# Kernel tuning notes

Hardware: AMD Instinct MI355X
Metric: run time of the kernel (lower is better)

Reference implementation:

```python
import jax, jax.numpy as jnp
import numpy as np

NC = 65536   # candidate centers across FPN levels (single image)
NP = 1024    # proposal boxes == points
D = 256      # points_feat_dim
C = 256      # in_channels (query/key dim)
START_LEVEL = 3
NEG = -1e30


def setup_inputs() -> dict:
    key = jax.random.key(0)
    ks = jax.random.split(key, 9)
    # centers: [y, x, size, stride]; stride in {8,16,32,64,128} -> lvl 0..4
    lvl = jax.random.randint(ks[0], (NC,), 0, 5)
    stride = (2.0 ** (lvl + START_LEVEL)).astype(jnp.float32)
    yx = jax.random.uniform(ks[1], (NC, 2), minval=0.0, maxval=1024.0)
    centers = jnp.concatenate([yx, stride[:, None], stride[:, None]], axis=1)
    # boxes: [x1, y1, x2, y2]
    x1y1 = jax.random.uniform(ks[2], (NP, 2), minval=0.0, maxval=900.0)
    wh = jax.random.uniform(ks[3], (NP, 2), minval=64.0, maxval=256.0)
    boxes = jnp.concatenate([x1y1, x1y1 + wh], axis=1)
    points_feat = jax.random.normal(ks[4], (NP, D), dtype=jnp.float32)
    box_feat = jax.random.normal(ks[5], (NC, D), dtype=jnp.float32)
    Wq = jax.random.normal(ks[6], (D, C), dtype=jnp.float32) / np.sqrt(D).astype(np.float32)
    bq = jnp.zeros((C,), dtype=jnp.float32)
    Wk = jax.random.normal(ks[7], (D, C), dtype=jnp.float32) / np.sqrt(D).astype(np.float32)
    bk = jnp.zeros((C,), dtype=jnp.float32)
    scales = 1.0 + 0.1 * jax.random.normal(ks[8], (5,), dtype=jnp.float32)
    return dict(points_feat=points_feat, box_feat=box_feat, centers=centers,
                boxes=boxes, Wq=Wq, bq=bq, Wk=Wk, bk=bk, scales=scales)


def reference(points_feat, box_feat, centers, boxes, Wq, bq, Wk, bk, scales):
    # geometry -> containment mask [NC, NP] (center c inside box p)
    coord = centers[:, :2] + jnp.floor_divide(centers[:, 2:3], 2.0)  # [NC,2]
    ys, xs = coord[:, 0], coord[:, 1]
    l = xs[:, None] - boxes[None, :, 0]
    t = ys[:, None] - boxes[None, :, 1]
    r = boxes[None, :, 2] - xs[:, None]
    b = boxes[None, :, 3] - ys[:, None]
    mask = jnp.minimum(jnp.minimum(l, t), jnp.minimum(r, b)) > 0     # [NC,NP]

    stride = centers[:, 3]
    lvl = (jnp.log2(stride) - START_LEVEL).astype(jnp.int32)         # [NC] in 0..4
    w = scales[lvl]                                                  # per-level scale

    query = points_feat @ Wq + bq                                    # [NP,C]
    keyf = (box_feat * w[:, None]) @ Wk + bk                         # [NC,C]

    sim = jnp.clip(keyf @ query.T, -50.0, 50.0)                      # [NC,NP]
    logits = jnp.where(mask, sim, NEG)
    attn = jax.nn.softmax(logits, axis=0)
    attn = jnp.where(mask, attn, 0.0)                                # zero out invalid
    merge = attn.T @ box_feat                                        # [NP,D]
    return points_feat + merge
```

## Files before the change

### kernel.cpp

```cpp
#include <hip/hip_runtime.h>

typedef unsigned short ushort_t;
typedef _Float16 half8 __attribute__((ext_vector_type(8)));
typedef short short8 __attribute__((ext_vector_type(8)));
typedef float floatx4 __attribute__((ext_vector_type(4)));

#define NCC 65536
#define NPP 1024
#define DD 256
#define NCHUNK 64
#define VROW 36
#define VTILE_B (256 * VROW * 2)

static __device__ __forceinline__ ushort_t f2h_bits(float x) {
  _Float16 h = (_Float16)x;
  return __builtin_bit_cast(ushort_t, h);
}
static __device__ __forceinline__ ushort_t f2bf_bits(float x) {
  unsigned u = __builtin_bit_cast(unsigned, x);
  unsigned r = (u + 0x7FFFu + ((u >> 16) & 1u)) >> 16;
  return (ushort_t)r;
}
static __device__ __forceinline__ ushort_t f2bf_cast(float x) {
  __bf16 h = (__bf16)x;
  return __builtin_bit_cast(ushort_t, h);
}

static __device__ __forceinline__ void dma16(const void* g, void* l) {
  __builtin_amdgcn_global_load_lds((const __attribute__((address_space(1))) unsigned int*)g,
                                   (__attribute__((address_space(3))) unsigned int*)l, 16, 0, 0);
}

static __device__ __forceinline__ short8 mk_s8(uint2 lo, uint2 hi) {
  uint4 u;
  u.x = lo.x; u.y = lo.y; u.z = hi.x; u.w = hi.y;
  return __builtin_bit_cast(short8, u);
}

__global__ __launch_bounds__(256) void wt_prep(const float* __restrict__ Wq,
                                               const float* __restrict__ Wk,
                                               ushort_t* __restrict__ WqT,
                                               ushort_t* __restrict__ WkT) {
  __shared__ __align__(16) ushort_t lt[64][80];
  const float* W = blockIdx.y ? Wk : Wq;
  ushort_t* WT = blockIdx.y ? WkT : WqT;
  const int k0 = ((int)blockIdx.x & 3) * 64, n0 = ((int)blockIdx.x >> 2) * 64;
  const int t = threadIdx.x;
#pragma unroll
  for (int i = 0; i < 4; i++) {
    int f = t + 256 * i;
    int k = f >> 4, j = (f & 15) * 4;
    const float4 v = *(const float4*)&W[(size_t)(k0 + k) * DD + n0 + j];
    lt[j + 0][k] = f2h_bits(v.x);
    lt[j + 1][k] = f2h_bits(v.y);
    lt[j + 2][k] = f2h_bits(v.z);
    lt[j + 3][k] = f2h_bits(v.w);
  }
  __syncthreads();
#pragma unroll
  for (int i = 0; i < 2; i++) {
    int f = t + 256 * i;
    int nl = f >> 3, grp = f & 7;
    int n = n0 + nl;
    int kp = k0 + ((grp ^ (n & 7)) * 8);
    *(uint4*)&WT[(size_t)n * DD + kp] = *(const uint4*)&lt[nl][grp * 8];
  }
}

__global__ __launch_bounds__(256) void prep_gemm(
    const float* __restrict__ box_feat, const float* __restrict__ points_feat,
    const float* __restrict__ centers, const float* __restrict__ scales,
    const ushort_t* __restrict__ WqT, const ushort_t* __restrict__ WkT,
    const float* __restrict__ bq, const float* __restrict__ bk,
    ushort_t* __restrict__ q_out, ushort_t* __restrict__ kf_out,
    ushort_t* __restrict__ vTb, float2* __restrict__ xy) {
  __shared__ __align__(16) ushort_t lds_a[64][264];
  __shared__ __align__(16) ushort_t lds_b[64 * 256];
  __shared__ __align__(16) ushort_t lds_o[64][72];
  __shared__ float lds_s[64];

  const int t = threadIdx.x;
  const bool isQ = (blockIdx.x >= (NCC / 64));
  const int row0 = isQ ? ((int)blockIdx.x - NCC / 64) * 64 : (int)blockIdx.x * 64;
  const float* In = isQ ? points_feat : box_feat;
  const ushort_t* WT = isQ ? WqT : WkT;
  const float* Bi = isQ ? bq : bk;
  ushort_t* Out = isQ ? q_out : kf_out;
  const int swz = isQ ? 0 : 7;

  const int r0 = t >> 4;
  const int cj = (t & 15) * 4;
  float4 vld[4][4];
#pragma unroll
  for (int p = 0; p < 4; ++p)
#pragma unroll
    for (int i2 = 0; i2 < 4; ++i2)
      vld[p][i2] = *(const float4*)&In[(size_t)(row0 + r0 + 16 * i2) * DD + p * 64 + cj];

  if (t < 64) {
    float s = 1.0f;
    if (!isQ) {
      int c = row0 + t;
      float stride = centers[c * 4 + 3];
      int lvl = (int)(log2f(stride) + 0.5f) - 3;
      lvl = lvl < 0 ? 0 : (lvl > 4 ? 4 : lvl);
      s = scales[lvl];
      float hf = floorf(centers[c * 4 + 2] * 0.5f);
      xy[c] = make_float2(centers[c * 4 + 1] + hf, centers[c * 4 + 0] + hf);
    }
    lds_s[t] = s;
  }
  __syncthreads();

  float sc[4];
#pragma unroll
  for (int i2 = 0; i2 < 4; ++i2) sc[i2] = lds_s[r0 + 16 * i2];

  {
    ushort_t(*lt)[72] = lds_o;
#pragma unroll
    for (int p = 0; p < 4; ++p) {
#pragma unroll
      for (int i2 = 0; i2 < 4; ++i2) {
        const float4 v = vld[p][i2];
        const int row = r0 + 16 * i2;
        const float s = sc[i2];
        ushort_t h0 = f2h_bits(v.x * s), h1 = f2h_bits(v.y * s);
        ushort_t h2 = f2h_bits(v.z * s), h3 = f2h_bits(v.w * s);
        *(uint2*)&lds_a[row][p * 64 + cj] =
            make_uint2((unsigned)h0 | ((unsigned)h1 << 16), (unsigned)h2 | ((unsigned)h3 << 16));
        if (!isQ) {
          lt[cj + 0][row] = f2bf_bits(v.x);
          lt[cj + 1][row] = f2bf_bits(v.y);
          lt[cj + 2][row] = f2bf_bits(v.z);
          lt[cj + 3][row] = f2bf_bits(v.w);
        }
      }
      if (!isQ) {
        __syncthreads();
#pragma unroll
        for (int i3 = 0; i3 < 2; i3++) {
          int f = t + 256 * i3;
          int d = f >> 3, jg = f & 7;
          int tile = (row0 >> 5) + (jg >> 2);
          size_t ob = (size_t)tile * (256 * VROW) + (size_t)(p * 64 + d) * VROW + (jg & 3) * 8;
          const uint2* src = (const uint2*)&lt[d][jg * 8];
          *(uint2*)&vTb[ob] = src[0];
          *(uint2*)&vTb[ob + 4] = src[1];
        }
        __syncthreads();
      }
    }
  }

  const int w = t >> 6, lane = t & 63, qd = lane >> 4, n = lane & 15;
  const int sw8 = (n & 7) * 8;

  for (int g = 0; g < 4; ++g) {
    __syncthreads();
#pragma unroll
    for (int j = 0; j < 8; ++j) {
      int sg = w * 8 + j;
      dma16(&WT[(size_t)g * 64 * DD + sg * 512 + lane * 8], &lds_b[sg * 512 + lane * 8]);
    }
    __syncthreads();

    floatx4 acc[4] = {};
#pragma unroll
    for (int s = 0; s < 8; s++) {
      half8 af = __builtin_bit_cast(half8, *(const uint4*)&lds_a[w * 16 + n][s * 32 + qd * 8]);
      int off = (s * 32 + qd * 8) ^ sw8;
#pragma unroll
      for (int nt = 0; nt < 4; ++nt) {
        half8 bf = __builtin_bit_cast(half8, *(const uint4*)&lds_b[(nt * 16 + n) * 256 + off]);
        acc[nt] = __builtin_amdgcn_mfma_f32_16x16x32_f16(af, bf, acc[nt], 0, 0, 0);
      }
    }
#pragma unroll
    for (int nt = 0; nt < 4; ++nt) {
      float b = Bi[g * 64 + nt * 16 + n];
#pragma unroll
      for (int r = 0; r < 4; r++) lds_o[w * 16 + qd * 4 + r][nt * 16 + n] = f2h_bits(acc[nt][r] + b);
    }
    __syncthreads();
#pragma unroll
    for (int i = 0; i < 2; i++) {
      int idx = t * 2 + i;
      int r = idx >> 3, grp = idx & 7;
      uint4 v = *(const uint4*)&lds_o[r][grp * 8];
      int grpS = grp ^ (swz & (r & 7));
      *(uint4*)&Out[(size_t)(row0 + r) * DD + (g * 8 + grpS) * 8] = v;
    }
  }
}

template <bool PART>
__global__ __launch_bounds__(256, 2) void attn_kernel(
    const ushort_t* __restrict__ qf16, const ushort_t* __restrict__ kf16,
    const ushort_t* __restrict__ vTb, const float2* __restrict__ xy,
    const float* __restrict__ boxes, float* __restrict__ acc_out,
    float* __restrict__ den_out) {
  __shared__ __align__(16) ushort_t lds_k[2][32 * 256];
  __shared__ __align__(16) ushort_t lds_v[2][256 * VROW];
  __shared__ __align__(16) ushort_t lds_p[4][32][VROW];

  const int t = threadIdx.x;
  const int w = t >> 6, lane = t & 63, qd = lane >> 4, n = lane & 15;
  const int chunk = blockIdx.x;
  const int p0w = blockIdx.y * 128 + w * 32;
  const int cchunk = chunk * 1024;
  const int sw16 = (n & 7) * 16;

  half8 qfr[2][8];
  float4 bxv[2];
#pragma unroll
  for (int pt = 0; pt < 2; ++pt) {
    int p = p0w + pt * 16 + n;
#pragma unroll
    for (int s = 0; s < 8; s++)
      qfr[pt][s] =
          __builtin_bit_cast(half8, *(const uint4*)&qf16[(size_t)p * DD + s * 32 + qd * 8]);
    bxv[pt] = *(const float4*)&boxes[p * 4];
  }

  floatx4 macc[2][16] = {};
  float dsum0 = 0.f, dsum1 = 0.f;

  auto stage = [&](int it, int buf) {
    const size_t kbase = (size_t)(cchunk + it * 32) * DD * 2;
#pragma unroll
    for (int j = 0; j < 4; ++j) {
      int i = w * 4 + j;
      dma16((const char*)kf16 + kbase + i * 1024 + lane * 16,
            (char*)lds_k[buf] + i * 1024 + lane * 16);
    }
    const size_t vbase = (size_t)((cchunk >> 5) + it) * VTILE_B;
#pragma unroll
    for (int j = 0; j < 4; ++j) {
      int i = j * 4 + w;
      dma16((const char*)vTb + vbase + i * 1024 + lane * 16,
            (char*)lds_v[buf] + i * 1024 + lane * 16);
    }
    if (w < 2) {
      int i = 16 + w;
      dma16((const char*)vTb + vbase + i * 1024 + lane * 16,
            (char*)lds_v[buf] + i * 1024 + lane * 16);
    }
  };

  stage(0, 0);

  for (int it = 0; it < 32; ++it) {
    const int buf = it & 1;
    const int cb = cchunk + it * 32;
    __syncthreads();
    if (it + 1 < 32) stage(it + 1, buf ^ 1);

#pragma unroll
    for (int t2 = 0; t2 < 2; ++t2) {
      const char* krow = (const char*)lds_k[buf] + (t2 * 16 + n) * 512;
      floatx4 a0 = {}, a1 = {};
#pragma unroll
      for (int s = 0; s < 8; s++) {
        half8 af = __builtin_bit_cast(half8, *(const uint4*)(krow + ((s * 64 + qd * 16) ^ sw16)));
        a0 = __builtin_amdgcn_mfma_f32_16x16x32_f16(af, qfr[0][s], a0, 0, 0, 0);
        a1 = __builtin_amdgcn_mfma_f32_16x16x32_f16(af, qfr[1][s], a1, 0, 0, 0);
      }
      unsigned pk00 = 0, pk01 = 0, pk10 = 0, pk11 = 0;
#pragma unroll
      for (int r = 0; r < 4; r++) {
        int cl = t2 * 16 + qd * 4 + r;
        float2 pxy = xy[cb + cl];
        {
          float mn = fminf(fminf(pxy.x - bxv[0].x, pxy.y - bxv[0].y),
                           fminf(bxv[0].z - pxy.x, bxv[0].w - pxy.y));
          float sim = __builtin_amdgcn_fmed3f(a0[r], -50.f, 50.f);
          float e = (mn > 0.f) ? __builtin_amdgcn_exp2f((sim - 50.f) * 1.44269504f) : 0.f;
          dsum0 += e;
          unsigned b = (unsigned)f2bf_cast(e);
          if (r == 0) pk00 = b;
          else if (r == 1) pk00 |= b << 16;
          else if (r == 2) pk01 = b;
          else pk01 |= b << 16;
        }
        {
          float mn = fminf(fminf(pxy.x - bxv[1].x, pxy.y - bxv[1].y),
                           fminf(bxv[1].z - pxy.x, bxv[1].w - pxy.y));
          float sim = __builtin_amdgcn_fmed3f(a1[r], -50.f, 50.f);
          float e = (mn > 0.f) ? __builtin_amdgcn_exp2f((sim - 50.f) * 1.44269504f) : 0.f;
          dsum1 += e;
          unsigned b = (unsigned)f2bf_cast(e);
          if (r == 0) pk10 = b;
          else if (r == 1) pk10 |= b << 16;
          else if (r == 2) pk11 = b;
          else pk11 |= b << 16;
        }
      }
      *(uint2*)&lds_p[w][n][t2 * 16 + qd * 4] = make_uint2(pk00, pk01);
      *(uint2*)&lds_p[w][16 + n][t2 * 16 + qd * 4] = make_uint2(pk10, pk11);
    }
    __asm__ volatile("s_waitcnt lgkmcnt(0)" ::: "memory");

    const char* pr0 = (const char*)&lds_p[w][n][0];
    const char* pr1 = (const char*)&lds_p[w][16 + n][0];
    short8 a20 = mk_s8(*(const uint2*)(pr0 + qd * 16), *(const uint2*)(pr0 + qd * 16 + 8));
    short8 a21 = mk_s8(*(const uint2*)(pr1 + qd * 16), *(const uint2*)(pr1 + qd * 16 + 8));
#pragma unroll
    for (int dt = 0; dt < 16; ++dt) {
      const char* vrow = (const char*)lds_v[buf] + (dt * 16 + n) * (VROW * 2);
      short8 b2 = mk_s8(*(const uint2*)(vrow + qd * 16), *(const uint2*)(vrow + qd * 16 + 8));
      macc[0][dt] = __builtin_amdgcn_mfma_f32_16x16x32_bf16(a20, b2, macc[0][dt], 0, 0, 0);
      macc[1][dt] = __builtin_amdgcn_mfma_f32_16x16x32_bf16(a21, b2, macc[1][dt], 0, 0, 0);
    }
  }

  dsum0 += __shfl_xor(dsum0, 16, 64);
  dsum0 += __shfl_xor(dsum0, 32, 64);
  dsum1 += __shfl_xor(dsum1, 16, 64);
  dsum1 += __shfl_xor(dsum1, 32, 64);

  if (PART) {
    if (lane < 16) {
      den_out[(size_t)chunk * NPP + p0w + n] = dsum0;
      den_out[(size_t)chunk * NPP + p0w + 16 + n] = dsum1;
    }
    float* ab = acc_out + (size_t)chunk * NPP * DD;
#pragma unroll
    for (int pt = 0; pt < 2; ++pt)
#pragma unroll
      for (int dt = 0; dt < 16; ++dt)
#pragma unroll
        for (int r = 0; r < 4; r++)
          ab[(size_t)(p0w + pt * 16 + qd * 4 + r) * DD + dt * 16 + n] = macc[pt][dt][r];
  } else {
    if (lane < 16) {
      atomicAdd(&den_out[p0w + n], dsum0);
      atomicAdd(&den_out[p0w + 16 + n], dsum1);
    }
#pragma unroll
    for (int pt = 0; pt < 2; ++pt)
#pragma unroll
      for (int dt = 0; dt < 16; ++dt)
#pragma unroll
        for (int r = 0; r < 4; r++)
          atomicAdd(&acc_out[(size_t)(p0w + pt * 16 + qd * 4 + r) * DD + dt * 16 + n],
                    macc[pt][dt][r]);
  }
}

__global__ __launch_bounds__(256) void reduce_finalize(const float* __restrict__ points_feat,
                                                       const float* __restrict__ acc_part,
                                                       const float* __restrict__ den_part,
                                                       float* __restrict__ out) {
  const int p = blockIdx.x, t = threadIdx.x;
  float s = 0.f;
#pragma unroll 4
  for (int c = 0; c < NCHUNK; ++c) s += acc_part[((size_t)c * NPP + p) * DD + t];
  float dn = den_part[(size_t)(t & 63) * NPP + p];
#pragma unroll
  for (int o = 1; o < 64; o <<= 1) dn += __shfl_xor(dn, o, 64);
  float m = (dn > 0.f) ? s / dn : 0.f;
  out[(size_t)p * DD + t] = points_feat[(size_t)p * DD + t] + m;
}

__global__ void finalize(const float* __restrict__ points_feat, const float* __restrict__ acc,
                         const float* __restrict__ den, float* __restrict__ out) {
  int p = blockIdx.x, d = threadIdx.x;
  float dn = den[p];
  float m = (dn > 0.f) ? acc[p * DD + d] / dn : 0.f;
  out[p * DD + d] = points_feat[p * DD + d] + m;
}

extern "C" void kernel_launch(void* const* d_in, const int* in_sizes, int n_in, void* d_out,
                              int out_size, void* d_ws, size_t ws_size, hipStream_t stream) {
  const float* points_feat = (const float*)d_in[0];
  const float* box_feat = (const float*)d_in[1];
  const float* centers = (const float*)d_in[2];
  const float* boxes = (const float*)d_in[3];
  const float* Wq = (const float*)d_in[4];
  const float* bq = (const float*)d_in[5];
  const float* Wk = (const float*)d_in[6];
  const float* bk = (const float*)d_in[7];
  const float* scales = (const float*)d_in[8];

  char* p = (char*)d_ws;
  ushort_t* ws_q = (ushort_t*)p;        p += (size_t)NPP * DD * 2;
  ushort_t* ws_kf = (ushort_t*)p;       p += (size_t)NCC * DD * 2;
  ushort_t* ws_vTb = (ushort_t*)p;      p += (size_t)(NCC / 32) * VTILE_B;
  float2* ws_xy = (float2*)p;           p += (size_t)NCC * 8;
  ushort_t* ws_wqT = (ushort_t*)p;      p += (size_t)DD * DD * 2;
  ushort_t* ws_wkT = (ushort_t*)p;      p += (size_t)DD * DD * 2;
  float* ws_den = (float*)p;            p += (size_t)NCHUNK * NPP * 4;
  float* ws_acc = (float*)p;
  size_t need_part = (size_t)(p - (char*)d_ws) + (size_t)NCHUNK * NPP * DD * 4;
  const bool part = ws_size >= need_part;

  wt_prep<<<dim3(16, 2), 256, 0, stream>>>(Wq, Wk, ws_wqT, ws_wkT);
  prep_gemm<<<NCC / 64 + NPP / 64, 256, 0, stream>>>(box_feat, points_feat, centers, scales,
                                                     ws_wqT, ws_wkT, bq, bk, ws_q, ws_kf,
                                                     ws_vTb, ws_xy);
  if (part) {
    attn_kernel<true><<<dim3(NCHUNK, 8), 256, 0, stream>>>(ws_q, ws_kf, ws_vTb, ws_xy, boxes,
                                                           ws_acc, ws_den);
    reduce_finalize<<<NPP, 256, 0, stream>>>(points_feat, ws_acc, ws_den, (float*)d_out);
  } else {
    hipMemsetAsync(ws_den, 0, ((size_t)NPP * DD + NPP) * sizeof(float), stream);
    float* acc1 = ws_den + NPP;
    attn_kernel<false><<<dim3(NCHUNK, 8), 256, 0, stream>>>(ws_q, ws_kf, ws_vTb, ws_xy, boxes,
                                                            acc1, ws_den);
    finalize<<<NPP, DD, 0, stream>>>(points_feat, acc1, ws_den, (float*)d_out);
  }
}
```

Before: 268.2 us.

## Split Q projection into small front-scheduled blocks and prefetch Wk tiles early

The query projection moves into 128 small blocks placed at the start of the grid, each computing 16 rows by 128 columns, replacing 16 large trailing blocks that ran at the end of the grid. In the key blocks, the first Wk tile is now issued before the feature loads, and each later Wk tile is issued right after the previous tile's results are staged, so weight loading overlaps the transpose and output stores. The goal is a shorter tail for the prep kernel and less time waiting on weight DMA, at the cost of more blocks and some duplicate weight traffic.

```diff
diff --git a/kernel.cpp b/kernel.cpp
--- a/kernel.cpp
+++ b/kernel.cpp
@@ -9,6 +9,7 @@
 #define NPP 1024
 #define DD 256
 #define NCHUNK 64
+#define NQMICRO 128
 #define VROW 36
 #define VTILE_B (256 * VROW * 2)
 
@@ -80,13 +81,67 @@
   __shared__ float lds_s[64];
 
   const int t = threadIdx.x;
-  const bool isQ = (blockIdx.x >= (NCC / 64));
-  const int row0 = isQ ? ((int)blockIdx.x - NCC / 64) * 64 : (int)blockIdx.x * 64;
-  const float* In = isQ ? points_feat : box_feat;
-  const ushort_t* WT = isQ ? WqT : WkT;
-  const float* Bi = isQ ? bq : bk;
-  ushort_t* Out = isQ ? q_out : kf_out;
-  const int swz = isQ ? 0 : 7;
+  const int w = t >> 6, lane = t & 63, qd = lane >> 4, n = lane & 15;
+  const int sw8 = (n & 7) * 8;
+
+  if (blockIdx.x < NQMICRO) {
+    const int m = (int)blockIdx.x;
+    const int qrow0 = (m >> 1) * 16;
+    const int gbase = (m & 1) * 2;
+#pragma unroll
+    for (int j = 0; j < 8; ++j) {
+      int sg = w * 8 + j;
+      dma16(&WqT[(size_t)gbase * 64 * DD + sg * 512 + lane * 8], &lds_b[sg * 512 + lane * 8]);
+    }
+#pragma unroll
+    for (int q = 0; q < 4; ++q) {
+      const float4 v =
+          *(const float4*)&points_feat[(size_t)(qrow0 + (t >> 4)) * DD + (t & 15) * 16 + q * 4];
+      ushort_t h0 = f2h_bits(v.x), h1 = f2h_bits(v.y);
+      ushort_t h2 = f2h_bits(v.z), h3 = f2h_bits(v.w);
+      *(uint2*)&lds_a[t >> 4][(t & 15) * 16 + q * 4] =
+          make_uint2((unsigned)h0 | ((unsigned)h1 << 16), (unsigned)h2 | ((unsigned)h3 << 16));
+    }
+#pragma unroll
+    for (int gi = 0; gi < 2; ++gi) {
+      const int g = gbase + gi;
+      __syncthreads();
+      floatx4 acc = {};
+#pragma unroll
+      for (int s = 0; s < 8; s++) {
+        half8 af = __builtin_bit_cast(half8, *(const uint4*)&lds_a[n][s * 32 + qd * 8]);
+        int off = (s * 32 + qd * 8) ^ sw8;
+        half8 bf = __builtin_bit_cast(half8, *(const uint4*)&lds_b[(w * 16 + n) * 256 + off]);
+        acc = __builtin_amdgcn_mfma_f32_16x16x32_f16(af, bf, acc, 0, 0, 0);
+      }
+      float b = bq[g * 64 + w * 16 + n];
+#pragma unroll
+      for (int r = 0; r < 4; r++) lds_o[qd * 4 + r][w * 16 + n] = f2h_bits(acc[r] + b);
+      __syncthreads();
+      if (gi == 0) {
+#pragma unroll
+        for (int j = 0; j < 8; ++j) {
+          int sg = w * 8 + j;
+          dma16(&WqT[(size_t)(gbase + 1) * 64 * DD + sg * 512 + lane * 8],
+                &lds_b[sg * 512 + lane * 8]);
+        }
+      }
+      if (t < 128) {
+        int r = t >> 3, grp = t & 7;
+        uint4 v = *(const uint4*)&lds_o[r][grp * 8];
+        *(uint4*)&q_out[(size_t)(qrow0 + r) * DD + (g * 8 + grp) * 8] = v;
+      }
+    }
+    return;
+  }
+
+  const int row0 = ((int)blockIdx.x - NQMICRO) * 64;
+
+#pragma unroll
+  for (int j = 0; j < 8; ++j) {
+    int sg = w * 8 + j;
+    dma16(&WkT[(size_t)sg * 512 + lane * 8], &lds_b[sg * 512 + lane * 8]);
+  }
 
   const int r0 = t >> 4;
   const int cj = (t & 15) * 4;
@@ -95,19 +150,16 @@
   for (int p = 0; p < 4; ++p)
 #pragma unroll
     for (int i2 = 0; i2 < 4; ++i2)
-      vld[p][i2] = *(const float4*)&In[(size_t)(row0 + r0 + 16 * i2) * DD + p * 64 + cj];
+      vld[p][i2] = *(const float4*)&box_feat[(size_t)(row0 + r0 + 16 * i2) * DD + p * 64 + cj];
 
   if (t < 64) {
-    float s = 1.0f;
-    if (!isQ) {
-      int c = row0 + t;
-      float stride = centers[c * 4 + 3];
-      int lvl = (int)(log2f(stride) + 0.5f) - 3;
-      lvl = lvl < 0 ? 0 : (lvl > 4 ? 4 : lvl);
-      s = scales[lvl];
-      float hf = floorf(centers[c * 4 + 2] * 0.5f);
-      xy[c] = make_float2(centers[c * 4 + 1] + hf, centers[c * 4 + 0] + hf);
-    }
+    int c = row0 + t;
+    float stride = centers[c * 4 + 3];
+    int lvl = (int)(log2f(stride) + 0.5f) - 3;
+    lvl = lvl < 0 ? 0 : (lvl > 4 ? 4 : lvl);
+    float s = scales[lvl];
+    float hf = floorf(centers[c * 4 + 2] * 0.5f);
+    xy[c] = make_float2(centers[c * 4 + 1] + hf, centers[c * 4 + 0] + hf);
     lds_s[t] = s;
   }
   __syncthreads();
@@ -129,42 +181,28 @@
         ushort_t h2 = f2h_bits(v.z * s), h3 = f2h_bits(v.w * s);
         *(uint2*)&lds_a[row][p * 64 + cj] =
             make_uint2((unsigned)h0 | ((unsigned)h1 << 16), (unsigned)h2 | ((unsigned)h3 << 16));
-        if (!isQ) {
-          lt[cj + 0][row] = f2bf_bits(v.x);
-          lt[cj + 1][row] = f2bf_bits(v.y);
-          lt[cj + 2][row] = f2bf_bits(v.z);
-          lt[cj + 3][row] = f2bf_bits(v.w);
-        }
-      }
-      if (!isQ) {
-        __syncthreads();
-#pragma unroll
-        for (int i3 = 0; i3 < 2; i3++) {
-          int f = t + 256 * i3;
-          int d = f >> 3, jg = f & 7;
-          int tile = (row0 >> 5) + (jg >> 2);
-          size_t ob = (size_t)tile * (256 * VROW) + (size_t)(p * 64 + d) * VROW + (jg & 3) * 8;
-          const uint2* src = (const uint2*)&lt[d][jg * 8];
-          *(uint2*)&vTb[ob] = src[0];
-          *(uint2*)&vTb[ob + 4] = src[1];
-        }
-        __syncthreads();
-      }
-    }
-  }
-
-  const int w = t >> 6, lane = t & 63, qd = lane >> 4, n = lane & 15;
-  const int sw8 = (n & 7) * 8;
+        lt[cj + 0][row] = f2bf_bits(v.x);
+        lt[cj + 1][row] = f2bf_bits(v.y);
+        lt[cj + 2][row] = f2bf_bits(v.z);
+        lt[cj + 3][row] = f2bf_bits(v.w);
+      }
+      __syncthreads();
+#pragma unroll
+      for (int i3 = 0; i3 < 2; i3++) {
+        int f = t + 256 * i3;
+        int d = f >> 3, jg = f & 7;
+        int tile = (row0 >> 5) + (jg >> 2);
+        size_t ob = (size_t)tile * (256 * VROW) + (size_t)(p * 64 + d) * VROW + (jg & 3) * 8;
+        const uint2* src = (const uint2*)&lt[d][jg * 8];
+        *(uint2*)&vTb[ob] = src[0];
+        *(uint2*)&vTb[ob + 4] = src[1];
+      }
+      __syncthreads();
+    }
+  }
 
   for (int g = 0; g < 4; ++g) {
     __syncthreads();
-#pragma unroll
-    for (int j = 0; j < 8; ++j) {
-      int sg = w * 8 + j;
-      dma16(&WT[(size_t)g * 64 * DD + sg * 512 + lane * 8], &lds_b[sg * 512 + lane * 8]);
-    }
-    __syncthreads();
-
     floatx4 acc[4] = {};
 #pragma unroll
     for (int s = 0; s < 8; s++) {
@@ -178,18 +216,25 @@
     }
 #pragma unroll
     for (int nt = 0; nt < 4; ++nt) {
-      float b = Bi[g * 64 + nt * 16 + n];
+      float b = bk[g * 64 + nt * 16 + n];
 #pragma unroll
       for (int r = 0; r < 4; r++) lds_o[w * 16 + qd * 4 + r][nt * 16 + n] = f2h_bits(acc[nt][r] + b);
     }
     __syncthreads();
+    if (g < 3) {
+#pragma unroll
+      for (int j = 0; j < 8; ++j) {
+        int sg = w * 8 + j;
+        dma16(&WkT[(size_t)(g + 1) * 64 * DD + sg * 512 + lane * 8], &lds_b[sg * 512 + lane * 8]);
+      }
+    }
 #pragma unroll
     for (int i = 0; i < 2; i++) {
       int idx = t * 2 + i;
       int r = idx >> 3, grp = idx & 7;
       uint4 v = *(const uint4*)&lds_o[r][grp * 8];
-      int grpS = grp ^ (swz & (r & 7));
-      *(uint4*)&Out[(size_t)(row0 + r) * DD + (g * 8 + grpS) * 8] = v;
+      int grpS = grp ^ (7 & (r & 7));
+      *(uint4*)&kf_out[(size_t)(row0 + r) * DD + (g * 8 + grpS) * 8] = v;
     }
   }
 }
@@ -396,9 +441,9 @@
   const bool part = ws_size >= need_part;
 
   wt_prep<<<dim3(16, 2), 256, 0, stream>>>(Wq, Wk, ws_wqT, ws_wkT);
-  prep_gemm<<<NCC / 64 + NPP / 64, 256, 0, stream>>>(box_feat, points_feat, centers, scales,
-                                                     ws_wqT, ws_wkT, bq, bk, ws_q, ws_kf,
-                                                     ws_vTb, ws_xy);
+  prep_gemm<<<NQMICRO + NCC / 64, 256, 0, stream>>>(box_feat, points_feat, centers, scales,
+                                                    ws_wqT, ws_wkT, bq, bk, ws_q, ws_kf,
+                                                    ws_vTb, ws_xy);
   if (part) {
     attn_kernel<true><<<dim3(NCHUNK, 8), 256, 0, stream>>>(ws_q, ws_kf, ws_vTb, ws_xy, boxes,
                                                            ws_acc, ws_den);
```

Result: faster. 259.5 us (median of 2 runs) (-3.2%).
